# Kernel optimization log

Measured on AMD Instinct MI355X. Metric: run time of the kernel, lower is better.

## Reference

```python
import jax, jax.numpy as jnp
import numpy as np

N_DST = 25000
E = 400000
DN = 128   # dim_node
DE = 128   # dim_edge
DT = 128   # dim_time
DO = 128   # dim_out
H = 2      # num_head


def setup_inputs() -> dict:
    key = jax.random.key(0)
    ks = jax.random.split(key, 10)
    sc = 0.05
    node_h = jax.random.normal(ks[0], (N_DST + E, DN), jnp.float32)
    edge_f = jax.random.normal(ks[1], (E, DE), jnp.float32)
    dt = jax.random.uniform(ks[2], (E,), jnp.float32) * 100.0
    dst_idx = jax.random.randint(ks[3], (E,), 0, N_DST)
    # TimeEncode: Linear(1, dim_time) with w initialized to 1/10**linspace(0,9)
    time_w = jnp.asarray(1.0 / 10 ** np.linspace(0, 9, DT, dtype=np.float32))
    time_b = jnp.zeros((DT,), jnp.float32)
    Wq = jax.random.normal(ks[4], (DO, DN + DT), jnp.float32) * sc
    bq = jnp.zeros((DO,), jnp.float32)
    Wk = jax.random.normal(ks[5], (DO, DN + DE + DT), jnp.float32) * sc
    bk = jnp.zeros((DO,), jnp.float32)
    Wv = jax.random.normal(ks[6], (DO, DN + DE + DT), jnp.float32) * sc
    bv = jnp.zeros((DO,), jnp.float32)
    Wout = jax.random.normal(ks[7], (DO, DN + DO), jnp.float32) * sc
    bout = jnp.zeros((DO,), jnp.float32)
    gamma = jnp.ones((DO,), jnp.float32)
    beta = jnp.zeros((DO,), jnp.float32)
    return dict(node_h=node_h, edge_f=edge_f, dt=dt, dst_idx=dst_idx,
                time_w=time_w, time_b=time_b, Wq=Wq, bq=bq, Wk=Wk, bk=bk,
                Wv=Wv, bv=bv, Wout=Wout, bout=bout, gamma=gamma, beta=beta)


def reference(node_h, edge_f, dt, dst_idx, time_w, time_b,
              Wq, bq, Wk, bk, Wv, bv, Wout, bout, gamma, beta):
    num_dst = node_h.shape[0] - edge_f.shape[0]
    num_edges = edge_f.shape[0]
    tgt = node_h[:num_dst]            # [N, DN] target node embeddings
    src = node_h[num_dst:]            # [E, DN] per-edge source embeddings

    # TimeEncode: cos(w * dt + b)
    time_feats = jnp.cos(dt[:, None] * time_w[None, :] + time_b)          # [E, DT]
    zero_time = jnp.broadcast_to(jnp.cos(time_b), (num_dst, time_b.shape[0]))

    Qn = jnp.concatenate([tgt, zero_time], axis=1) @ Wq.T + bq            # [N, DO]
    kv_in = jnp.concatenate([src, edge_f, time_feats], axis=1)            # [E, DN+DE+DT]
    K = kv_in @ Wk.T + bk                                                 # [E, DO]
    V = kv_in @ Wv.T + bv                                                 # [E, DO]
    Q = Qn[dst_idx]                                                       # gather per edge

    d_head = Q.shape[1] // H
    Qh = Q.reshape(num_edges, H, d_head)
    Kh = K.reshape(num_edges, H, d_head)
    Vh = V.reshape(num_edges, H, d_head)

    score = jnp.sum(Qh * Kh, axis=2)                                      # [E, H]
    score = jnp.where(score >= 0, score, 0.2 * score)                     # LeakyReLU(0.2)

    # edge_softmax: segmented softmax over incoming edges of each dst node
    m = jax.ops.segment_max(score, dst_idx, num_segments=num_dst)
    m = jnp.where(jnp.isfinite(m), m, 0.0)                                # empty segments
    e = jnp.exp(score - m[dst_idx])
    s = jax.ops.segment_sum(e, dst_idx, num_segments=num_dst)
    att = e / s[dst_idx]                                                  # [E, H]

    Vw = (Vh * att[:, :, None]).reshape(num_edges, -1)                    # [E, DO]
    h = jax.ops.segment_sum(Vw, dst_idx, num_segments=num_dst)            # scatter-sum

    rst = jnp.concatenate([h, tgt], axis=1) @ Wout.T + bout               # [N, DO]
    rst = jax.nn.relu(rst)
    mu = jnp.mean(rst, axis=-1, keepdims=True)
    var = jnp.var(rst, axis=-1, keepdims=True)
    return (rst - mu) / jnp.sqrt(var + 1e-5) * gamma + beta
```

## Files before the change

kernel.cpp:

```cpp
#include <hip/hip_runtime.h>

#define N_DST 25000
#define E_NUM 400000

typedef __bf16 bf16x8 __attribute__((ext_vector_type(8)));
typedef __bf16 bf16x4 __attribute__((ext_vector_type(4)));
typedef __bf16 bf16x2 __attribute__((ext_vector_type(2)));
typedef float  f32x4  __attribute__((ext_vector_type(4)));

__device__ __forceinline__ float fast_cos(float x) {
  float r = x * 0.15915494309189535f;
  r = r - floorf(r);
  return __builtin_amdgcn_cosf(r);
}

__device__ __forceinline__ void gload_lds16(const void* g, void* l) {
  __builtin_amdgcn_global_load_lds(
      (const __attribute__((address_space(1))) unsigned int*)g,
      (__attribute__((address_space(3))) unsigned int*)l, 16, 0, 0);
}

__device__ __forceinline__ void pack_frag(const float* __restrict__ W0,
    const float* __restrict__ W1, int stride, int NC, int idx, __bf16* __restrict__ out) {
  int lane = idx & 63, fid = idx >> 6;
  int nfw = NC >> 6;
  int perks = nfw << 2;
  int ks = fid / perks, rem = fid - ks * perks;
  int w = rem / nfw, nf = rem - w * nfw;
  int n = w * (NC >> 2) + nf * 16 + (lane & 15);
  int g = (ks << 2) + (lane >> 4);
  const float* src = (W1 && n >= 128) ? (W1 + (size_t)(n - 128) * stride)
                                      : (W0 + (size_t)n * stride);
  const float4* s4 = reinterpret_cast<const float4*>(src + g * 8);
  float4 lo = s4[0], hi = s4[1];
  bf16x8 b;
  b[0]=(__bf16)lo.x; b[1]=(__bf16)lo.y; b[2]=(__bf16)lo.z; b[3]=(__bf16)lo.w;
  b[4]=(__bf16)hi.x; b[5]=(__bf16)hi.y; b[6]=(__bf16)hi.z; b[7]=(__bf16)hi.w;
  reinterpret_cast<bf16x8*>(out)[idx] = b;
}

__global__ __launch_bounds__(256) void prep_kernel(
    const float* __restrict__ Wq, const float* __restrict__ bq, const float* __restrict__ tb,
    const float* __restrict__ Wk, const float* __restrict__ Wv, const float* __restrict__ Wout,
    const int* __restrict__ dsti,
    float* __restrict__ cq, __bf16* __restrict__ Bq_kv, __bf16* __restrict__ Bq_q,
    __bf16* __restrict__ Bq_out, int* __restrict__ counts) {
  int b = blockIdx.x, tid = threadIdx.x;
  if (b == 0) {
    if (tid < 128) {
      float s = bq[tid];
      for (int j = 0; j < 128; ++j) s += cosf(tb[j]) * Wq[tid * 256 + 128 + j];
      cq[tid] = s;
    }
    return;
  }
  b -= 1;
  if (b < 48) { pack_frag(Wk, Wv, 384, 256, b * 256 + tid, Bq_kv); return; }
  b -= 48;
  if (b < 8)  { pack_frag(Wq, nullptr, 256, 128, b * 256 + tid, Bq_q); return; }
  b -= 8;
  if (b < 16) { pack_frag(Wout, nullptr, 256, 128, b * 256 + tid, Bq_out); return; }
  b -= 16;
  int e = b * 256 + tid;
  if (e < E_NUM) atomicAdd(&counts[dsti[e]], 1);
}

__global__ __launch_bounds__(1024) void scan_kernel(const int* __restrict__ counts,
    int* __restrict__ offs, int* __restrict__ cursor) {
  __shared__ int wpart[16];
  int tid = threadIdx.x, lane = tid & 63, wid = tid >> 6;
  int carry = 0;
  for (int base = 0; base < N_DST; base += 1024) {
    int idx = base + tid;
    int x = (idx < N_DST) ? counts[idx] : 0;
    int incl = x;
#pragma unroll
    for (int o = 1; o < 64; o <<= 1) {
      int y = __shfl_up(incl, o);
      if (lane >= o) incl += y;
    }
    if (lane == 63) wpart[wid] = incl;
    __syncthreads();
    if (wid == 0) {
      int v = (lane < 16) ? wpart[lane] : 0;
      int s = v;
#pragma unroll
      for (int o = 1; o < 16; o <<= 1) {
        int y = __shfl_up(s, o);
        if (lane >= o) s += y;
      }
      if (lane < 16) wpart[lane] = s;
    }
    __syncthreads();
    int woff = (wid > 0) ? wpart[wid - 1] : 0;
    int tot = wpart[15];
    if (idx < N_DST) {
      int v = carry + woff + incl - x;
      offs[idx] = v;
      cursor[idx] = v;
    }
    carry += tot;
    __syncthreads();
  }
  if (tid == 0) offs[N_DST] = carry;
}

__global__ __launch_bounds__(256) void fill_kernel(const int* __restrict__ dsti,
    int* __restrict__ cursor, int* __restrict__ elist, int* __restrict__ dsts) {
  int e = blockIdx.x * 256 + threadIdx.x;
  if (e < E_NUM) {
    int d = dsti[e];
    int p = atomicAdd(&cursor[d], 1);
    elist[p] = e;
    dsts[p] = d;
  }
}

__global__ __launch_bounds__(256, 4) void kv_kernel(
    const float* __restrict__ node_h, const float* __restrict__ edge_f,
    const float* __restrict__ dtp, const float* __restrict__ tw, const float* __restrict__ tb,
    const __bf16* __restrict__ Bq,
    const float* __restrict__ bk, const float* __restrict__ bv,
    const int* __restrict__ elist, const int* __restrict__ dsts,
    const float* __restrict__ Qn,
    __bf16* __restrict__ Vout, float* __restrict__ score)
{
  __shared__ __align__(16) float Abuf[2][4096];
  __shared__ int Elds[64];
  __shared__ int Dlds[64];
  __shared__ float dts[64];
  __shared__ float twl[128];
  __shared__ float tbl[128];

  const int tid = threadIdx.x;
  const int e0 = blockIdx.x * 64;
  const int lane = tid & 63;
  const int w = tid >> 6;
  const int lrow = lane & 15;
  const int lk = lane >> 4;
  const int aswz = (lrow & 7) << 4;

  if (tid < 64) {
    int e = elist[e0 + tid];
    Elds[tid] = e;
    Dlds[tid] = dsts[e0 + tid];
    dts[tid] = dtp[e];
  } else if (tid < 192) {
    int j = tid - 64;
    twl[j] = tw[j];
    tbl[j] = tb[j];
  }
  __syncthreads();

  auto stage_mem = [&](int t, int bufi) {
    const float* base;
    int coloff;
    if (t < 2) { base = node_h + (size_t)N_DST * 128; coloff = t * 64; }
    else       { base = edge_f;                       coloff = (t - 2) * 64; }
#pragma unroll
    for (int i = 0; i < 4; ++i) {
      int g = w * 4 + i;
      int r = g * 4 + (lane >> 4);
      const float* src = base + (size_t)Elds[r] * 128 + coloff;
      int boff = ((lane & 15) << 4) ^ ((r & 7) << 4);
      gload_lds16((const char*)src + boff, &Abuf[bufi][g * 256]);
    }
  };
  auto stage_cos = [&](int t, float* buf) {
    int r = tid >> 2;
    int j0 = (tid & 3) << 4;
    float d = dts[r];
    int swz = (r & 7) << 4;
    char* rowb = (char*)(buf + r * 64);
#pragma unroll
    for (int q = 0; q < 4; ++q) {
      f32x4 vv;
#pragma unroll
      for (int jj = 0; jj < 4; ++jj) {
        int J = (t - 4) * 64 + j0 + q * 4 + jj;
        vv[jj] = fast_cos(d * twl[J] + tbl[J]);
      }
      *reinterpret_cast<f32x4*>(rowb + (((j0 << 2) + (q << 4)) ^ swz)) = vv;
    }
  };

  f32x4 acc[4][4];
#pragma unroll
  for (int mf = 0; mf < 4; ++mf)
#pragma unroll
    for (int nf = 0; nf < 4; ++nf)
      acc[mf][nf] = (f32x4){0.f, 0.f, 0.f, 0.f};

  const bf16x8* __restrict__ Bw = reinterpret_cast<const bf16x8*>(Bq) + (size_t)(w * 4) * 64 + lane;

  auto ktile = [&](const float* buf, int t) {
#pragma unroll
    for (int ks = 0; ks < 2; ++ks) {
      int K32 = t * 2 + ks;
      bf16x8 b[4];
#pragma unroll
      for (int nf = 0; nf < 4; ++nf)
        b[nf] = Bw[((size_t)K32 * 16 + nf) * 64];
      bf16x8 a[4];
#pragma unroll
      for (int mf = 0; mf < 4; ++mf) {
        const char* rowb = (const char*)(buf + (mf * 16 + lrow) * 64);
        int cb = ks * 128 + lk * 32;
        f32x4 f0 = *reinterpret_cast<const f32x4*>(rowb + (cb ^ aswz));
        f32x4 f1 = *reinterpret_cast<const f32x4*>(rowb + ((cb + 16) ^ aswz));
        bf16x8 av;
#pragma unroll
        for (int j = 0; j < 4; ++j) {
          av[j] = (__bf16)f0[j];
          av[4 + j] = (__bf16)f1[j];
        }
        a[mf] = av;
      }
#pragma unroll
      for (int nf = 0; nf < 4; ++nf)
#pragma unroll
        for (int mf = 0; mf < 4; ++mf)
          acc[mf][nf] = __builtin_amdgcn_mfma_f32_16x16x32_bf16(a[mf], b[nf], acc[mf][nf], 0, 0, 0);
    }
  };

  stage_mem(0, 0);
  __syncthreads();
#pragma unroll
  for (int t = 0; t < 6; ++t) {
    if (t < 3) stage_mem(t + 1, (t + 1) & 1);
    else if (t < 5) stage_cos(t + 1, Abuf[(t + 1) & 1]);
    ktile(Abuf[t & 1], t);
    __syncthreads();
  }

  char* Vlds = (char*)Abuf[0];
  if (w >= 2) {
#pragma unroll
    for (int nf = 0; nf < 4; ++nf) {
      int vcol = (w - 2) * 64 + nf * 16 + lrow;
      float bb = bv[vcol];
#pragma unroll
      for (int mf = 0; mf < 4; ++mf) {
#pragma unroll
        for (int r = 0; r < 4; ++r) {
          int row = mf * 16 + lk * 4 + r;
          *reinterpret_cast<__bf16*>(Vlds + row * 256 + ((vcol * 2) ^ ((row & 7) << 4))) =
              (__bf16)(acc[mf][nf][r] + bb);
        }
      }
    }
  } else {
    float bkv[4];
#pragma unroll
    for (int nf = 0; nf < 4; ++nf) bkv[nf] = bk[w * 64 + nf * 16 + lrow];
#pragma unroll
    for (int mf = 0; mf < 4; ++mf) {
#pragma unroll
      for (int r = 0; r < 4; ++r) {
        int row = mf * 16 + lk * 4 + r;
        const float* qrow = Qn + ((size_t)Dlds[row] << 7) + w * 64;
        float s = 0.f;
#pragma unroll
        for (int nf = 0; nf < 4; ++nf)
          s += (acc[mf][nf][r] + bkv[nf]) * qrow[nf * 16 + lrow];
        s += __shfl_xor(s, 1);
        s += __shfl_xor(s, 2);
        s += __shfl_xor(s, 4);
        s += __shfl_xor(s, 8);
        if (lrow == 0) {
          s = (s >= 0.f) ? s : 0.2f * s;
          score[((size_t)(e0 + row) << 1) + w] = s;
        }
      }
    }
  }
  __syncthreads();
#pragma unroll
  for (int i = 0; i < 4; ++i) {
    int c = tid + i * 256;
    int r = c >> 4, cb = (c & 15) << 4;
    bf16x8 vv = *reinterpret_cast<const bf16x8*>(Vlds + r * 256 + (cb ^ ((r & 7) << 4)));
    *reinterpret_cast<bf16x8*>(Vout + (((size_t)(e0 + r)) << 7) + (c & 15) * 8) = vv;
  }
}

template<int MODE>
__global__ __launch_bounds__(256, 4) void gemm_kernel(
    const float* __restrict__ A0, const float* __restrict__ A1,
    const float* __restrict__ dtp, const float* __restrict__ tw,
    const __bf16* __restrict__ Bq, const float* __restrict__ bias0,
    float* __restrict__ outF)
{
  constexpr int NC = 128;
  constexpr int NFRAGW = 2;
  __shared__ __align__(16) char Abuf[2][64 * 256];

  const int tid = threadIdx.x;
  const int e0 = blockIdx.x * 64;
  const int nv = min(64, N_DST - e0);
  const int srow = tid >> 5;
  const int sc4 = (tid & 31) << 2;

  const int lane = tid & 63;
  const int w = tid >> 6;
  const int nbase = w * (NC / 4);
  const int lrow = lane & 15;
  const int lk = lane >> 4;
  const int aswz = (lrow & 7) << 4;
  const bf16x8* __restrict__ Bw =
      reinterpret_cast<const bf16x8*>(Bq) + (size_t)(w * NFRAGW) * 64 + lane;

  f32x4 acc[4][NFRAGW];
#pragma unroll
  for (int mf = 0; mf < 4; ++mf)
#pragma unroll
    for (int nf = 0; nf < NFRAGW; ++nf)
      acc[mf][nf] = (f32x4){0.f, 0.f, 0.f, 0.f};

  auto issueA = [&](int t, float4 (&v)[8]) {
    const float* base = (t == 0) ? A0 : A1;
#pragma unroll
    for (int i = 0; i < 8; ++i) {
      int r = srow + i * 8;
      v[i] = (r < nv) ? *reinterpret_cast<const float4*>(base + (size_t)(e0 + r) * 128 + sc4)
                      : make_float4(0.f, 0.f, 0.f, 0.f);
    }
  };
  auto writeA = [&](char* buf, float4 (&v)[8]) {
#pragma unroll
    for (int i = 0; i < 8; ++i) {
      int r = srow + i * 8;
      bf16x4 b;
      b[0]=(__bf16)v[i].x; b[1]=(__bf16)v[i].y; b[2]=(__bf16)v[i].z; b[3]=(__bf16)v[i].w;
      *reinterpret_cast<bf16x4*>(buf + r * 256 + ((sc4 * 2) ^ ((r & 7) << 4))) = b;
    }
  };
  auto ktile = [&](const char* buf, int t) {
#pragma unroll
    for (int ks = 0; ks < 4; ++ks) {
      bf16x8 b[NFRAGW];
#pragma unroll
      for (int nf = 0; nf < NFRAGW; ++nf)
        b[nf] = Bw[((size_t)(t * 4 + ks) * 4 * NFRAGW + nf) * 64];
      bf16x8 a[4];
#pragma unroll
      for (int mf = 0; mf < 4; ++mf)
        a[mf] = *reinterpret_cast<const bf16x8*>(
            buf + (mf * 16 + lrow) * 256 + (((ks * 32 + lk * 8) * 2) ^ aswz));
#pragma unroll
      for (int nf = 0; nf < NFRAGW; ++nf)
#pragma unroll
        for (int mf = 0; mf < 4; ++mf)
          acc[mf][nf] = __builtin_amdgcn_mfma_f32_16x16x32_bf16(a[mf], b[nf], acc[mf][nf], 0, 0, 0);
    }
  };

  float4 v[8];
  issueA(0, v);
  writeA(Abuf[0], v);
  __syncthreads();
  if constexpr (MODE == 2) {
    issueA(1, v);
    ktile(Abuf[0], 0);
    writeA(Abuf[1], v);
    __syncthreads();
    ktile(Abuf[1], 1);
  } else {
    ktile(Abuf[0], 0);
  }

  if constexpr (MODE == 0) {
#pragma unroll
    for (int nf = 0; nf < NFRAGW; ++nf) {
      int col = nbase + nf * 16 + lrow;
      float bb = bias0[col];
#pragma unroll
      for (int mf = 0; mf < 4; ++mf) {
#pragma unroll
        for (int r = 0; r < 4; ++r) {
          int row = mf * 16 + lk * 4 + r;
          if (row < nv)
            outF[(size_t)(e0 + row) * 128 + col] = acc[mf][nf][r] + bb;
        }
      }
    }
  } else {
    const float* gammaP = dtp;
    const float* betaP = tw;
    float vals[NFRAGW][4][4];
#pragma unroll
    for (int nf = 0; nf < NFRAGW; ++nf) {
      float bb = bias0[nbase + nf * 16 + lrow];
#pragma unroll
      for (int mf = 0; mf < 4; ++mf)
#pragma unroll
        for (int r = 0; r < 4; ++r)
          vals[nf][mf][r] = fmaxf(acc[mf][nf][r] + bb, 0.f);
    }
    __syncthreads();
    float* sums = reinterpret_cast<float*>(Abuf[0]);
    float* sqs  = reinterpret_cast<float*>(Abuf[0]) + 256;
    float* stats = reinterpret_cast<float*>(Abuf[0]) + 512;
#pragma unroll
    for (int mf = 0; mf < 4; ++mf) {
#pragma unroll
      for (int r = 0; r < 4; ++r) {
        float s1 = vals[0][mf][r] + vals[1][mf][r];
        float s2 = vals[0][mf][r] * vals[0][mf][r] + vals[1][mf][r] * vals[1][mf][r];
#pragma unroll
        for (int o = 1; o < 16; o <<= 1) {
          s1 += __shfl_xor(s1, o);
          s2 += __shfl_xor(s2, o);
        }
        if (lrow == 0) {
          int row = mf * 16 + lk * 4 + r;
          sums[w * 64 + row] = s1;
          sqs[w * 64 + row] = s2;
        }
      }
    }
    __syncthreads();
    if (tid < 64) {
      float s = sums[tid] + sums[64 + tid] + sums[128 + tid] + sums[192 + tid];
      float q = sqs[tid] + sqs[64 + tid] + sqs[128 + tid] + sqs[192 + tid];
      float mean = s * (1.f / 128.f);
      float var = q * (1.f / 128.f) - mean * mean;
      stats[tid * 2] = mean;
      stats[tid * 2 + 1] = rsqrtf(var + 1e-5f);
    }
    __syncthreads();
#pragma unroll
    for (int nf = 0; nf < NFRAGW; ++nf) {
      int col = nbase + nf * 16 + lrow;
      float g = gammaP[col], bC = betaP[col];
#pragma unroll
      for (int mf = 0; mf < 4; ++mf) {
#pragma unroll
        for (int r = 0; r < 4; ++r) {
          int row = mf * 16 + lk * 4 + r;
          if (row < nv) {
            float mean = stats[row * 2], rs = stats[row * 2 + 1];
            outF[(size_t)(e0 + row) * 128 + col] = (vals[nf][mf][r] - mean) * rs * g + bC;
          }
        }
      }
    }
  }
}

__global__ __launch_bounds__(256) void agg_kernel(const int* __restrict__ offs,
    const float* __restrict__ score, const __bf16* __restrict__ V, float* __restrict__ h) {
  int d = blockIdx.x * 4 + (threadIdx.x >> 6);
  if (d >= N_DST) return;
  int lane = threadIdx.x & 63;
  int beg = offs[d], end = offs[d + 1];
  int n = end - beg;
  float m0 = -3.0e38f, m1 = -3.0e38f;
  for (int i = lane; i < n; i += 64) {
    float2 sc = *reinterpret_cast<const float2*>(score + 2 * (size_t)(beg + i));
    m0 = fmaxf(m0, sc.x); m1 = fmaxf(m1, sc.y);
  }
#pragma unroll
  for (int o = 32; o; o >>= 1) {
    m0 = fmaxf(m0, __shfl_xor(m0, o));
    m1 = fmaxf(m1, __shfl_xor(m1, o));
  }
  float s0 = 0.f, s1 = 0.f;
  for (int i = lane; i < n; i += 64) {
    float2 sc = *reinterpret_cast<const float2*>(score + 2 * (size_t)(beg + i));
    s0 += __expf(sc.x - m0); s1 += __expf(sc.y - m1);
  }
#pragma unroll
  for (int o = 32; o; o >>= 1) {
    s0 += __shfl_xor(s0, o);
    s1 += __shfl_xor(s1, o);
  }
  float inv0 = (n > 0) ? 1.f / s0 : 0.f;
  float inv1 = (n > 0) ? 1.f / s1 : 0.f;
  int q = lane >> 4, j = lane & 15;
  int hsel = j >> 3;
  float acc[8];
#pragma unroll
  for (int k2 = 0; k2 < 8; ++k2) acc[k2] = 0.f;
  for (int i0 = 0; i0 < n; i0 += 4) {
    int i = i0 + q;
    if (i < n) {
      size_t p = beg + i;
      float2 sc = *reinterpret_cast<const float2*>(score + 2 * p);
      float wgt = hsel ? __expf(sc.y - m1) * inv1 : __expf(sc.x - m0) * inv0;
      bf16x8 v = *reinterpret_cast<const bf16x8*>(V + (p << 7) + j * 8);
#pragma unroll
      for (int k2 = 0; k2 < 8; ++k2) acc[k2] += wgt * (float)v[k2];
    }
  }
#pragma unroll
  for (int k2 = 0; k2 < 8; ++k2) {
    acc[k2] += __shfl_xor(acc[k2], 16);
    acc[k2] += __shfl_xor(acc[k2], 32);
  }
  if (q == 0) {
    float4 lo = make_float4(acc[0], acc[1], acc[2], acc[3]);
    float4 hi = make_float4(acc[4], acc[5], acc[6], acc[7]);
    float* dst = h + ((size_t)d << 7) + j * 8;
    *reinterpret_cast<float4*>(dst) = lo;
    *reinterpret_cast<float4*>(dst + 4) = hi;
  }
}

extern "C" void kernel_launch(void* const* d_in, const int* in_sizes, int n_in,
                              void* d_out, int out_size, void* d_ws, size_t ws_size,
                              hipStream_t stream) {
  (void)in_sizes; (void)n_in; (void)out_size; (void)ws_size;
  const float* node_h = (const float*)d_in[0];
  const float* edge_f = (const float*)d_in[1];
  const float* dtp    = (const float*)d_in[2];
  const int*   dsti   = (const int*)d_in[3];
  const float* tw     = (const float*)d_in[4];
  const float* tb     = (const float*)d_in[5];
  const float* Wq     = (const float*)d_in[6];
  const float* bq     = (const float*)d_in[7];
  const float* Wk     = (const float*)d_in[8];
  const float* bk     = (const float*)d_in[9];
  const float* Wv     = (const float*)d_in[10];
  const float* bv     = (const float*)d_in[11];
  const float* Wout   = (const float*)d_in[12];
  const float* bout   = (const float*)d_in[13];
  const float* gamma  = (const float*)d_in[14];
  const float* beta   = (const float*)d_in[15];
  float* outp = (float*)d_out;

  size_t off = 0;
  auto take = [&](size_t nbytes) -> void* {
    void* r = (char*)d_ws + off;
    off += (nbytes + 255) & ~(size_t)255;
    return r;
  };
  __bf16* Bq_kv  = (__bf16*)take((size_t)12288 * 16);
  __bf16* Bq_q   = (__bf16*)take((size_t)2048 * 16);
  __bf16* Bq_out = (__bf16*)take((size_t)4096 * 16);
  float*  cq     = (float*)take(128 * 4);
  float*  Qn     = (float*)take((size_t)N_DST * 128 * 4);
  __bf16* Vbuf   = (__bf16*)take((size_t)E_NUM * 128 * 2);
  float*  score  = (float*)take((size_t)E_NUM * 2 * 4);
  int*    counts = (int*)take((size_t)N_DST * 4);
  int*    offs   = (int*)take((size_t)(N_DST + 1) * 4);
  int*    cursor = (int*)take((size_t)N_DST * 4);
  int*    elist  = (int*)take((size_t)E_NUM * 4);
  int*    dsts   = (int*)take((size_t)E_NUM * 4);
  float*  hbuf   = (float*)take((size_t)N_DST * 128 * 4);

  hipMemsetAsync(counts, 0, (size_t)N_DST * 4, stream);

  const int count_blocks = (E_NUM + 255) / 256;
  prep_kernel<<<1 + 48 + 8 + 16 + count_blocks, 256, 0, stream>>>(
      Wq, bq, tb, Wk, Wv, Wout, dsti, cq, Bq_kv, Bq_q, Bq_out, counts);

  gemm_kernel<0><<<(N_DST + 63) / 64, 256, 0, stream>>>(node_h, nullptr, nullptr, nullptr,
      Bq_q, cq, Qn);

  scan_kernel<<<1, 1024, 0, stream>>>(counts, offs, cursor);
  fill_kernel<<<count_blocks, 256, 0, stream>>>(dsti, cursor, elist, dsts);

  kv_kernel<<<E_NUM / 64, 256, 0, stream>>>(node_h, edge_f, dtp, tw, tb,
      Bq_kv, bk, bv, elist, dsts, Qn, Vbuf, score);

  agg_kernel<<<(N_DST + 3) / 4, 256, 0, stream>>>(offs, score, Vbuf, hbuf);

  gemm_kernel<2><<<(N_DST + 63) / 64, 256, 0, stream>>>(hbuf, node_h, gamma, beta,
      Bq_out, bout, outp);
}
```

Measured before the change: 364.8 us.

## Read edges in natural order and scatter outputs; deepen kv pipeline to three buffers

The kv kernel now reads source-node and edge features contiguously in original edge order instead of gathering them through a sorted edge list. The V and score outputs are scattered to their CSR positions via a per-edge position array, so fill_kernel writes only one array instead of two. The staging loop becomes a triple-buffered pipeline with explicit vmcnt waits and raw barriers in place of __syncthreads. This trades gathered 512-byte row reads for contiguous reads plus scattered 256-byte writes, and lowers the occupancy hint from 4 to 3 blocks because shared memory grows.

Result: no change. 360.2 us (-1.3%).

```diff
diff --git a/kernel.cpp b/kernel.cpp
--- a/kernel.cpp
+++ b/kernel.cpp
@@ -19,6 +19,15 @@
       (const __attribute__((address_space(1))) unsigned int*)g,
       (__attribute__((address_space(3))) unsigned int*)l, 16, 0, 0);
 }
+
+#define PIPE_WAIT(S)                         \
+  do {                                       \
+    __builtin_amdgcn_sched_barrier(0);       \
+    asm volatile(S ::: "memory");            \
+    __builtin_amdgcn_sched_barrier(0);       \
+    __builtin_amdgcn_s_barrier();            \
+    __builtin_amdgcn_sched_barrier(0);       \
+  } while (0)
 
 __device__ __forceinline__ void pack_frag(const float* __restrict__ W0,
     const float* __restrict__ W1, int stride, int NC, int idx, __bf16* __restrict__ out) {
@@ -106,28 +115,27 @@
 }
 
 __global__ __launch_bounds__(256) void fill_kernel(const int* __restrict__ dsti,
-    int* __restrict__ cursor, int* __restrict__ elist, int* __restrict__ dsts) {
+    int* __restrict__ cursor, int* __restrict__ pos) {
   int e = blockIdx.x * 256 + threadIdx.x;
   if (e < E_NUM) {
     int d = dsti[e];
     int p = atomicAdd(&cursor[d], 1);
-    elist[p] = e;
-    dsts[p] = d;
-  }
-}
-
-__global__ __launch_bounds__(256, 4) void kv_kernel(
+    pos[e] = p;
+  }
+}
+
+__global__ __launch_bounds__(256, 3) void kv_kernel(
     const float* __restrict__ node_h, const float* __restrict__ edge_f,
     const float* __restrict__ dtp, const float* __restrict__ tw, const float* __restrict__ tb,
     const __bf16* __restrict__ Bq,
     const float* __restrict__ bk, const float* __restrict__ bv,
-    const int* __restrict__ elist, const int* __restrict__ dsts,
+    const int* __restrict__ dsti, const int* __restrict__ pos,
     const float* __restrict__ Qn,
     __bf16* __restrict__ Vout, float* __restrict__ score)
 {
-  __shared__ __align__(16) float Abuf[2][4096];
-  __shared__ int Elds[64];
+  __shared__ __align__(16) float Abuf[3][4096];
   __shared__ int Dlds[64];
+  __shared__ int Plds[64];
   __shared__ float dts[64];
   __shared__ float twl[128];
   __shared__ float tbl[128];
@@ -141,10 +149,9 @@
   const int aswz = (lrow & 7) << 4;
 
   if (tid < 64) {
-    int e = elist[e0 + tid];
-    Elds[tid] = e;
-    Dlds[tid] = dsts[e0 + tid];
-    dts[tid] = dtp[e];
+    Dlds[tid] = dsti[e0 + tid];
+    Plds[tid] = pos[e0 + tid];
+    dts[tid] = dtp[e0 + tid];
   } else if (tid < 192) {
     int j = tid - 64;
     twl[j] = tw[j];
@@ -153,17 +160,15 @@
   __syncthreads();
 
   auto stage_mem = [&](int t, int bufi) {
-    const float* base;
-    int coloff;
-    if (t < 2) { base = node_h + (size_t)N_DST * 128; coloff = t * 64; }
-    else       { base = edge_f;                       coloff = (t - 2) * 64; }
+    const char* base;
+    if (t < 2) base = (const char*)(node_h + ((size_t)(N_DST + e0)) * 128 + t * 64);
+    else       base = (const char*)(edge_f + (size_t)e0 * 128 + (t - 2) * 64);
 #pragma unroll
     for (int i = 0; i < 4; ++i) {
       int g = w * 4 + i;
       int r = g * 4 + (lane >> 4);
-      const float* src = base + (size_t)Elds[r] * 128 + coloff;
-      int boff = ((lane & 15) << 4) ^ ((r & 7) << 4);
-      gload_lds16((const char*)src + boff, &Abuf[bufi][g * 256]);
+      int srcoff = r * 512 + ((((lane & 15) << 4)) ^ ((r & 7) << 4));
+      gload_lds16(base + srcoff, &Abuf[bufi][g * 256]);
     }
   };
   auto stage_cos = [&](int t, float* buf) {
@@ -225,14 +230,18 @@
   };
 
   stage_mem(0, 0);
-  __syncthreads();
-#pragma unroll
-  for (int t = 0; t < 6; ++t) {
-    if (t < 3) stage_mem(t + 1, (t + 1) & 1);
-    else if (t < 5) stage_cos(t + 1, Abuf[(t + 1) & 1]);
-    ktile(Abuf[t & 1], t);
-    __syncthreads();
-  }
+  stage_mem(1, 1);
+  PIPE_WAIT("s_waitcnt vmcnt(4)");
+  stage_mem(2, 2); ktile(Abuf[0], 0);
+  PIPE_WAIT("s_waitcnt vmcnt(4)");
+  stage_mem(3, 0); ktile(Abuf[1], 1);
+  PIPE_WAIT("s_waitcnt vmcnt(4)");
+  stage_cos(4, Abuf[1]); ktile(Abuf[2], 2);
+  PIPE_WAIT("s_waitcnt vmcnt(0) lgkmcnt(0)");
+  stage_cos(5, Abuf[2]); ktile(Abuf[0], 3);
+  PIPE_WAIT("s_waitcnt lgkmcnt(0)");
+  ktile(Abuf[1], 4);
+  ktile(Abuf[2], 5);
 
   char* Vlds = (char*)Abuf[0];
   if (w >= 2) {
@@ -270,7 +279,7 @@
         s += __shfl_xor(s, 8);
         if (lrow == 0) {
           s = (s >= 0.f) ? s : 0.2f * s;
-          score[((size_t)(e0 + row) << 1) + w] = s;
+          score[((size_t)Plds[row] << 1) + w] = s;
         }
       }
     }
@@ -281,7 +290,7 @@
     int c = tid + i * 256;
     int r = c >> 4, cb = (c & 15) << 4;
     bf16x8 vv = *reinterpret_cast<const bf16x8*>(Vlds + r * 256 + (cb ^ ((r & 7) << 4)));
-    *reinterpret_cast<bf16x8*>(Vout + (((size_t)(e0 + r)) << 7) + (c & 15) * 8) = vv;
+    *reinterpret_cast<bf16x8*>(Vout + (((size_t)Plds[r]) << 7) + (c & 15) * 8) = vv;
   }
 }
 
@@ -546,8 +555,7 @@
   int*    counts = (int*)take((size_t)N_DST * 4);
   int*    offs   = (int*)take((size_t)(N_DST + 1) * 4);
   int*    cursor = (int*)take((size_t)N_DST * 4);
-  int*    elist  = (int*)take((size_t)E_NUM * 4);
-  int*    dsts   = (int*)take((size_t)E_NUM * 4);
+  int*    pos    = (int*)take((size_t)E_NUM * 4);
   float*  hbuf   = (float*)take((size_t)N_DST * 128 * 4);
 
   hipMemsetAsync(counts, 0, (size_t)N_DST * 4, stream);
@@ -560,10 +568,10 @@
       Bq_q, cq, Qn);
 
   scan_kernel<<<1, 1024, 0, stream>>>(counts, offs, cursor);
-  fill_kernel<<<count_blocks, 256, 0, stream>>>(dsti, cursor, elist, dsts);
+  fill_kernel<<<count_blocks, 256, 0, stream>>>(dsti, cursor, pos);
 
   kv_kernel<<<E_NUM / 64, 256, 0, stream>>>(node_h, edge_f, dtp, tw, tb,
-      Bq_kv, bk, bv, elist, dsts, Qn, Vbuf, score);
+      Bq_kv, bk, bv, dsti, pos, Qn, Vbuf, score);
 
   agg_kernel<<<(N_DST + 3) / 4, 256, 0, stream>>>(offs, score, Vbuf, hbuf);
 
```
